# Kernel tuning notes

Measured on AMD Instinct MI355X. Metric: run time of the kernel, lower is better.

Reference implementation:

```python
import jax, jax.numpy as jnp
import numpy as np

T = 2048          # tokens (flattened batch*seq, vLLM style)
HID = 2048        # hidden_size
NH = 16           # num_heads
D_NOPE = 128
D_ROPE = 64
D_QK = D_NOPE + D_ROPE   # 192
D_V = 128
Q_LORA = 1536
KV_LORA = 512
THETA = 10000.0
EPS = 1e-6
SCALING = D_QK ** -0.5


def _rmsnorm(x, g):
    return x * jax.lax.rsqrt(jnp.mean(x * x, axis=-1, keepdims=True) + EPS) * g


def _rope(pos, x):
    # interleaved (is_neox_style=False) rotary embedding
    d = x.shape[-1]
    inv = 1.0 / (THETA ** (jnp.arange(0, d, 2, dtype=jnp.float32) / d))
    f = pos.astype(jnp.float32)[:, None] * inv          # [T, d/2]
    cos, sin = jnp.cos(f), jnp.sin(f)
    for _ in range(x.ndim - 2):                          # broadcast over heads
        cos, sin = cos[:, None], sin[:, None]
    x1, x2 = x[..., 0::2], x[..., 1::2]
    o1 = x1 * cos - x2 * sin
    o2 = x1 * sin + x2 * cos
    return jnp.stack([o1, o2], axis=-1).reshape(x.shape)


def setup_inputs() -> dict:
    key = jax.random.key(0)
    ks = jax.random.split(key, 6)
    s = 0.02
    return {
        "hidden_states": jax.random.normal(ks[0], (T, HID), jnp.float32),
        "positions": jnp.arange(T, dtype=jnp.int32),
        "w_qkv_a": jax.random.normal(ks[1], (HID, Q_LORA + KV_LORA + D_ROPE), jnp.float32) * s,
        "g_q": jnp.ones((Q_LORA,), jnp.float32),
        "w_q_b": jax.random.normal(ks[2], (Q_LORA, NH * D_QK), jnp.float32) * s,
        "g_kv": jnp.ones((KV_LORA,), jnp.float32),
        "w_kv_b": jax.random.normal(ks[3], (KV_LORA, NH * (D_NOPE + D_V)), jnp.float32) * s,
        "w_o": jax.random.normal(ks[4], (NH * D_V, HID), jnp.float32) * s,
    }


def reference(hidden_states, positions, w_qkv_a, g_q, w_q_b, g_kv, w_kv_b, w_o):
    # fused low-rank a-projection: [T, q_lora + kv_lora + rope]
    qkv_a = hidden_states @ w_qkv_a
    q_lat = qkv_a[:, :Q_LORA]
    kv_lat = qkv_a[:, Q_LORA:Q_LORA + KV_LORA]
    k_pe = qkv_a[:, Q_LORA + KV_LORA:]                   # [T, rope]

    # query path: rmsnorm -> b-projection -> [T, H, d_qk]
    q = (_rmsnorm(q_lat, g_q) @ w_q_b).reshape(T, NH, D_QK)
    q_nope, q_pe = q[..., :D_NOPE], q[..., D_NOPE:]

    # kv path: rmsnorm -> b-projection -> [T, H, nope + v]
    kv = (_rmsnorm(kv_lat, g_kv) @ w_kv_b).reshape(T, NH, D_NOPE + D_V)
    k_nope, v = kv[..., :D_NOPE], kv[..., D_NOPE:]

    q_pe = _rope(positions, q_pe)                        # [T, H, rope]
    k_pe = _rope(positions, k_pe)                        # [T, rope] shared MQA rope key

    qf = jnp.concatenate([q_nope, q_pe], axis=-1)        # [T, H, d_qk]
    kf = jnp.concatenate([k_nope, jnp.broadcast_to(k_pe[:, None, :], (T, NH, D_ROPE))], axis=-1)

    scores = jnp.einsum("thd,shd->hts", qf, kf) * SCALING   # [H, T, T]
    mask = jnp.tril(jnp.ones((T, T), dtype=bool))
    scores = jnp.where(mask, scores, jnp.finfo(scores.dtype).min)
    probs = jax.nn.softmax(scores, axis=-1)
    out = jnp.einsum("hts,shd->thd", probs, v)           # [T, H, d_v]
    return out.reshape(T, NH * D_V) @ w_o                # [T, hidden]
```

## Files before the change

### kernel.cpp

```cpp
#include <hip/hip_runtime.h>
#include <hip/hip_bf16.h>
#include <math.h>

typedef __bf16 bf16_t;
typedef __bf16 bf16x8 __attribute__((ext_vector_type(8)));
typedef float floatx4 __attribute__((ext_vector_type(4)));
typedef int intx4 __attribute__((ext_vector_type(4)));

#define T_TOK 2048
#define HID 2048
#define NH 16
#define D_NOPE 128
#define D_ROPE 64
#define D_QK 192
#define D_V 128
#define Q_LORA 1536
#define KV_LORA 512
#define QKV_N 2112
#define QKV_NPAD 2176
#define SCALING 0.07216878364870323f
#define LOG2E 1.442695041f
#define EXP_C1 (SCALING * LOG2E)
#define EXP_C2 (12.0f * LOG2E)

#define MFMA_BF16(a, b, c) __builtin_amdgcn_mfma_f32_16x16x32_bf16(a, b, c, 0, 0, 0)

__device__ __forceinline__ void gload16(const void* g, void* l) {
    __builtin_amdgcn_global_load_lds(
        (const __attribute__((address_space(1))) unsigned int*)g,
        (__attribute__((address_space(3))) unsigned int*)l, 16, 0, 0);
}

template <int MODE>
__device__ __forceinline__ void gemm_body(
    const bf16_t* __restrict__ A, const bf16_t* __restrict__ Bt,
    float* __restrict__ Cf, bf16_t* __restrict__ Cb,
    bf16_t* __restrict__ kfull, bf16_t* __restrict__ vT,
    int N, int K, int m0, int n0, bf16_t* S)
{
    bf16_t* As = S;
    bf16_t* Bs = S + 16384;
    const int tid = threadIdx.x;
    const int lane = tid & 63;
    const int w = tid >> 6;
    const int wm = w >> 1, wn = w & 1;
    const int l15 = lane & 15, quad = lane >> 4;
    const int ckey = (l15 >> 1) & 3;

    floatx4 acc[4][4] = {};

#define GSTAGE(db_, k0_)                                                                 \
    do {                                                                                 \
        _Pragma("unroll")                                                                \
        for (int it = 0; it < 4; ++it) {                                                 \
            int slot = it * 256 + tid;                                                   \
            int kk2 = slot >> 9;                                                         \
            int r = (slot >> 2) & 127;                                                   \
            int c = slot & 3;                                                            \
            int cs = c ^ ((r >> 1) & 3);                                                 \
            gload16((const char*)(A + (size_t)(m0 + r) * K + (k0_) + kk2 * 32 + cs * 8), \
                    (char*)(As + (size_t)(db_)*8192) + slot * 16);                       \
            gload16((const char*)(Bt + (size_t)(n0 + r) * K + (k0_) + kk2 * 32 + cs * 8),\
                    (char*)(Bs + (size_t)(db_)*8192) + slot * 16);                       \
        }                                                                                \
    } while (0)

    GSTAGE(0, 0);
    int db = 0;
    for (int k0 = 0; k0 < K; k0 += 64) {
        __syncthreads();
        if (k0 + 64 < K) GSTAGE(db ^ 1, k0 + 64);
        const bf16_t* Ab = As + (size_t)db * 8192;
        const bf16_t* Bb = Bs + (size_t)db * 8192;
#pragma unroll
        for (int kk2 = 0; kk2 < 2; ++kk2) {
            bf16x8 af[4], bfr[4];
#pragma unroll
            for (int mi = 0; mi < 4; ++mi)
                af[mi] = *(const bf16x8*)(Ab + kk2 * 4096 +
                                          (wm * 64 + mi * 16 + l15) * 32 +
                                          (quad ^ ckey) * 8);
#pragma unroll
            for (int ni = 0; ni < 4; ++ni)
                bfr[ni] = *(const bf16x8*)(Bb + kk2 * 4096 +
                                           (wn * 64 + ni * 16 + l15) * 32 +
                                           (quad ^ ckey) * 8);
#pragma unroll
            for (int mi = 0; mi < 4; ++mi)
#pragma unroll
                for (int ni = 0; ni < 4; ++ni)
                    acc[mi][ni] = MFMA_BF16(af[mi], bfr[ni], acc[mi][ni]);
        }
        db ^= 1;
    }
#undef GSTAGE

    if (MODE == 2) {
        const int hh = n0 >> 8;
        if ((n0 & 255) == 0) {
#pragma unroll
            for (int mi = 0; mi < 4; ++mi)
#pragma unroll
                for (int ni = 0; ni < 4; ++ni)
#pragma unroll
                    for (int r = 0; r < 4; ++r) {
                        int row = m0 + wm * 64 + mi * 16 + quad * 4 + r;
                        int dd = wn * 64 + ni * 16 + l15;
                        kfull[((size_t)hh * T_TOK + row) * 192 + dd] =
                            (bf16_t)acc[mi][ni][r];
                    }
        } else {
            __syncthreads();
            bf16_t* Tq = S;
#pragma unroll
            for (int mi = 0; mi < 4; ++mi)
#pragma unroll
                for (int ni = 0; ni < 4; ++ni)
#pragma unroll
                    for (int r = 0; r < 4; ++r) {
                        int rloc = wm * 64 + mi * 16 + quad * 4 + r;
                        int cloc = wn * 64 + ni * 16 + l15;
                        Tq[cloc * 136 + rloc] = (bf16_t)acc[mi][ni][r];
                    }
            __syncthreads();
#pragma unroll
            for (int pass = 0; pass < 8; ++pass) {
                int dcol = pass * 16 + w * 4 + quad;
                bf16x8 vv = *(const bf16x8*)(Tq + dcol * 136 + l15 * 8);
                *(bf16x8*)(vT + ((size_t)hh * 128 + dcol) * T_TOK + m0 + l15 * 8) = vv;
            }
        }
        return;
    }

#pragma unroll
    for (int mi = 0; mi < 4; ++mi)
#pragma unroll
        for (int ni = 0; ni < 4; ++ni)
#pragma unroll
            for (int r = 0; r < 4; ++r) {
                int row = m0 + wm * 64 + mi * 16 + quad * 4 + r;
                int col = n0 + wn * 64 + ni * 16 + l15;
                float v = acc[mi][ni][r];
                if (MODE == 1) {
                    Cb[(size_t)row * N + col] = (bf16_t)v;
                } else {
                    Cf[(size_t)row * N + col] = v;
                }
            }
}

template <int MODE>
__global__ __launch_bounds__(256) void gemm_mfma(
    const bf16_t* __restrict__ A, const bf16_t* __restrict__ Bt,
    float* __restrict__ Cf, bf16_t* __restrict__ Cb,
    bf16_t* __restrict__ kfull, bf16_t* __restrict__ vT,
    int M, int N, int K)
{
    __shared__ __align__(16) bf16_t S[4 * 8192];
    gemm_body<MODE>(A, Bt, Cf, Cb, kfull, vT, N, K,
                    blockIdx.y * 128, blockIdx.x * 128, S);
}

__global__ __launch_bounds__(256) void gemm_dual(
    const bf16_t* __restrict__ qn, const bf16_t* __restrict__ wqb,
    bf16_t* __restrict__ qbuf,
    const bf16_t* __restrict__ kvn, const bf16_t* __restrict__ wkvb,
    bf16_t* __restrict__ kfull, bf16_t* __restrict__ vT)
{
    __shared__ __align__(16) bf16_t S[4 * 8192];
    int id = blockIdx.x;
    if (id < 384) {
        gemm_body<1>(qn, wqb, nullptr, qbuf, nullptr, nullptr,
                     3072, Q_LORA, (id / 24) * 128, (id % 24) * 128, S);
    } else {
        int i2 = id - 384;
        gemm_body<2>(kvn, wkvb, nullptr, nullptr, kfull, vT,
                     4096, KV_LORA, (i2 / 32) * 128, (i2 % 32) * 128, S);
    }
}

__global__ void transpose_all(const float* __restrict__ w0, const float* __restrict__ w1,
                              const float* __restrict__ w2, const float* __restrict__ w3,
                              const float* __restrict__ hidden,
                              bf16_t* __restrict__ o0, bf16_t* __restrict__ o1,
                              bf16_t* __restrict__ o2, bf16_t* __restrict__ o3,
                              bf16_t* __restrict__ hbf) {
    int n0 = blockIdx.x * 32, k0 = blockIdx.y * 32;
    int tx = threadIdx.x, ty = threadIdx.y;
    if (blockIdx.z == 4) {
        if (n0 >= 2048 || k0 >= 2048) return;
        for (int i = ty; i < 32; i += 8)
            hbf[(size_t)(k0 + i) * 2048 + n0 + tx] =
                (bf16_t)hidden[(size_t)(k0 + i) * 2048 + n0 + tx];
        return;
    }
    const float* in; bf16_t* out; int K, N;
    switch (blockIdx.z) {
        case 0: in = w0; out = o0; K = 2048; N = 2112; break;
        case 1: in = w1; out = o1; K = 1536; N = 3072; break;
        case 2: in = w2; out = o2; K = 512;  N = 4096; break;
        default: in = w3; out = o3; K = 2048; N = 2048; break;
    }
    if (n0 >= N || k0 >= K) return;
    __shared__ float tile[32][33];
    for (int i = ty; i < 32; i += 8)
        tile[i][tx] = in[(size_t)(k0 + i) * N + n0 + tx];
    __syncthreads();
    for (int i = ty; i < 32; i += 8)
        out[(size_t)(n0 + i) * K + k0 + tx] = (bf16_t)tile[tx][i];
}

__global__ void mid_fuse(const float* __restrict__ qkv_a, const int* __restrict__ pos,
                         const float* __restrict__ g_q, const float* __restrict__ g_kv,
                         bf16_t* __restrict__ qn, bf16_t* __restrict__ kvn,
                         bf16_t* __restrict__ kfull, float2* __restrict__ ropet) {
    int t = blockIdx.x, tid = threadIdx.x;
    const float* x = qkv_a + (size_t)t * QKV_NPAD;
    __shared__ float red[256];
    float ss = 0.f;
    for (int c = tid; c < Q_LORA; c += 256) { float v = x[c]; ss += v * v; }
    red[tid] = ss;
    __syncthreads();
    for (int o = 128; o > 0; o >>= 1) {
        if (tid < o) red[tid] += red[tid + o];
        __syncthreads();
    }
    float rq = rsqrtf(red[0] / (float)Q_LORA + 1e-6f);
    __syncthreads();
    ss = 0.f;
    for (int c = Q_LORA + tid; c < Q_LORA + KV_LORA; c += 256) { float v = x[c]; ss += v * v; }
    red[tid] = ss;
    __syncthreads();
    for (int o = 128; o > 0; o >>= 1) {
        if (tid < o) red[tid] += red[tid + o];
        __syncthreads();
    }
    float rkv = rsqrtf(red[0] / (float)KV_LORA + 1e-6f);

    for (int c = tid; c < Q_LORA; c += 256)
        qn[(size_t)t * Q_LORA + c] = (bf16_t)(x[c] * rq * g_q[c]);
    for (int c = tid; c < KV_LORA; c += 256)
        kvn[(size_t)t * KV_LORA + c] = (bf16_t)(x[Q_LORA + c] * rkv * g_kv[c]);

    if (tid < 32) {
        int i = tid;
        double inv = pow(10000.0, -(double)(2 * i) / 64.0);
        double fd = (double)pos[t] * inv;
        float c = (float)cos(fd), s = (float)sin(fd);
        ropet[t * 32 + i] = make_float2(c, s);
        float x1 = x[Q_LORA + KV_LORA + 2 * i], x2 = x[Q_LORA + KV_LORA + 2 * i + 1];
        bf16_t v0 = (bf16_t)(x1 * c - x2 * s);
        bf16_t v1 = (bf16_t)(x1 * s + x2 * c);
#pragma unroll
        for (int h = 0; h < NH; ++h) {
            kfull[((size_t)h * T_TOK + t) * 192 + 128 + 2 * i] = v0;
            kfull[((size_t)h * T_TOK + t) * 192 + 128 + 2 * i + 1] = v1;
        }
    }
}

__global__ __launch_bounds__(256, 2) void attn_part(
    const bf16_t* __restrict__ qbuf, const bf16_t* __restrict__ kfull,
    const bf16_t* __restrict__ vT, const float2* __restrict__ ropet,
    bf16_t* __restrict__ oP0, bf16_t* __restrict__ oP1, float* __restrict__ l_part)
{
    const int id = blockIdx.x;
    const int h = id & 15;
    const int c = (id >> 4) & 3;
    const int qt = 15 - (id >> 6);
    const int q0 = qt * 128;
    const int nTile = 2 * (qt + 1);
    const int tbase = nTile >> 2, trem = nTile & 3;
    const int sz = tbase + (c < trem ? 1 : 0);
    const int sBeg = c * tbase + (c < trem ? c : trem);
    const int sEnd = sBeg + sz;
    const int unit = qt * 16 + h;
    const int tid = threadIdx.x, lane = tid & 63, w = tid >> 6;
    const int l15 = lane & 15, quad = lane >> 4;
    const int ckey = (l15 >> 1) & 3;

    __shared__ __align__(16) bf16_t kn2[2][6 * 64 * 32];
    __shared__ __align__(16) bf16_t vt2[2 * 128 * 32];
    __shared__ __align__(16) bf16_t p_s[128 * 64];

    bf16x8 qf[2][6];
#pragma unroll
    for (int st = 0; st < 2; ++st) {
        const bf16_t* qp = qbuf + (size_t)(q0 + w * 32 + st * 16 + l15) * (NH * D_QK) +
                           h * D_QK;
#pragma unroll
        for (int kk = 0; kk < 6; ++kk)
            qf[st][kk] = *(const bf16x8*)(qp + kk * 32 + quad * 8);
    }
#pragma unroll
    for (int st = 0; st < 2; ++st) {
        int t = q0 + w * 32 + st * 16 + l15;
#pragma unroll
        for (int kk = 4; kk < 6; ++kk)
#pragma unroll
            for (int p = 0; p < 4; ++p) {
                float2 cs = ropet[t * 32 + (kk - 4) * 16 + quad * 4 + p];
                float x1 = (float)qf[st][kk][2 * p], x2 = (float)qf[st][kk][2 * p + 1];
                qf[st][kk][2 * p] = (bf16_t)(x1 * cs.x - x2 * cs.y);
                qf[st][kk][2 * p + 1] = (bf16_t)(x1 * cs.y + x2 * cs.x);
            }
    }

    bf16x8 ones;
#pragma unroll
    for (int j = 0; j < 8; ++j) ones[j] = (bf16_t)1.0f;

    floatx4 o[2][8] = {};
    floatx4 lac[2] = {};
    intx4 vreg[4];

#define STAGE_KN(buf_, s0_)                                                              \
    do {                                                                                 \
        _Pragma("unroll")                                                                \
        for (int it = 0; it < 6; ++it) {                                                 \
            int slot = it * 256 + tid;                                                   \
            int kk = slot >> 8, s = (slot >> 2) & 63, cc = slot & 3;                     \
            int cs = cc ^ ((s >> 1) & 3);                                                \
            gload16((const char*)(kfull + ((size_t)h * T_TOK + (s0_) + s) * 192 +        \
                                  kk * 32 + cs * 8),                                     \
                    (char*)kn2[buf_] + slot * 16);                                       \
        }                                                                                \
    } while (0)

#define VLOAD(s0_)                                                                       \
    do {                                                                                 \
        _Pragma("unroll")                                                                \
        for (int it = 0; it < 4; ++it) {                                                 \
            int slot = it * 256 + tid;                                                   \
            int ks = slot >> 9, d = (slot >> 2) & 127, cc = slot & 3;                    \
            vreg[it] = *(const intx4*)(vT + ((size_t)h * 128 + d) * T_TOK + (s0_) +      \
                                       ks * 32 + cc * 8);                                \
        }                                                                                \
    } while (0)

#define VWRITE()                                                                         \
    do {                                                                                 \
        _Pragma("unroll")                                                                \
        for (int it = 0; it < 4; ++it) {                                                 \
            int slot = it * 256 + tid;                                                   \
            int ks = slot >> 9, d = (slot >> 2) & 127, cc = slot & 3;                    \
            *(intx4*)((char*)vt2 +                                                       \
                      (size_t)((ks * 512 + d * 4 + (cc ^ ((d >> 1) & 3))) * 16)) =       \
                vreg[it];                                                                \
        }                                                                                \
    } while (0)

    if (sz > 0) {
        VLOAD(sBeg * 64);
        STAGE_KN(0, sBeg * 64);
        VWRITE();
    }

    for (int si = sBeg; si < sEnd; ++si) {
        const int s0 = si * 64;
        const int buf = (si - sBeg) & 1;
        __syncthreads();
        if (si + 1 < sEnd) {
            VLOAD(s0 + 64);
            STAGE_KN(buf ^ 1, s0 + 64);
        }

        floatx4 s_acc[2][4] = {};
        __builtin_amdgcn_s_setprio(1);
#pragma unroll
        for (int ni = 0; ni < 4; ++ni) {
#pragma unroll
            for (int kk = 0; kk < 6; ++kk) {
                bf16x8 b = *(const bf16x8*)(kn2[buf] + kk * 2048 +
                                            (ni * 16 + l15) * 32 + (quad ^ ckey) * 8);
                s_acc[0][ni] = MFMA_BF16(qf[0][kk], b, s_acc[0][ni]);
                s_acc[1][ni] = MFMA_BF16(qf[1][kk], b, s_acc[1][ni]);
            }
        }
        __builtin_amdgcn_s_setprio(0);

        const bool diag = (si >= 2 * qt);
#pragma unroll
        for (int st = 0; st < 2; ++st)
#pragma unroll
            for (int ni = 0; ni < 4; ++ni)
#pragma unroll
                for (int r = 0; r < 4; ++r) {
                    int prow = w * 32 + st * 16 + quad * 4 + r;
                    int pcol = ni * 16 + l15;
                    float pv = exp2f(s_acc[st][ni][r] * EXP_C1 - EXP_C2);
                    if (diag && (s0 + pcol) > (q0 + prow)) pv = 0.f;
                    p_s[prow * 64 + ((((pcol >> 3) ^ (prow & 7))) << 3) + (pcol & 7)] =
                        (bf16_t)pv;
                }

        __builtin_amdgcn_s_setprio(1);
#pragma unroll
        for (int ks = 0; ks < 2; ++ks) {
            bf16x8 a0, a1;
            {
                int arow = w * 32 + l15;
                a0 = *(const bf16x8*)(p_s + arow * 64 +
                                      (((ks * 4 + quad) ^ (arow & 7)) << 3));
                arow += 16;
                a1 = *(const bf16x8*)(p_s + arow * 64 +
                                      (((ks * 4 + quad) ^ (arow & 7)) << 3));
            }
            lac[0] = MFMA_BF16(a0, ones, lac[0]);
            lac[1] = MFMA_BF16(a1, ones, lac[1]);
#pragma unroll
            for (int ni = 0; ni < 8; ++ni) {
                bf16x8 b = *(const bf16x8*)(vt2 + ks * 4096 +
                                            (ni * 16 + l15) * 32 + (quad ^ ckey) * 8);
                o[0][ni] = MFMA_BF16(a0, b, o[0][ni]);
                o[1][ni] = MFMA_BF16(a1, b, o[1][ni]);
            }
        }
        __builtin_amdgcn_s_setprio(0);

        __syncthreads();
        if (si + 1 < sEnd) VWRITE();
    }

    bf16_t* op = ((c < 2) ? oP0 : oP1) + (size_t)(unit * 2 + (c & 1)) * 128 * 128;
#pragma unroll
    for (int st = 0; st < 2; ++st) {
#pragma unroll
        for (int ni = 0; ni < 8; ++ni)
#pragma unroll
            for (int r = 0; r < 4; ++r) {
                int lrow = w * 32 + st * 16 + quad * 4 + r;
                op[(size_t)lrow * 128 + ni * 16 + l15] = (bf16_t)o[st][ni][r];
            }
        if (l15 == 0)
#pragma unroll
            for (int r = 0; r < 4; ++r) {
                int lrow = w * 32 + st * 16 + quad * 4 + r;
                l_part[((size_t)unit * 4 + c) * 128 + lrow] = lac[st][r];
            }
    }
#undef STAGE_KN
#undef VLOAD
#undef VWRITE
}

__global__ void attn_combine(const bf16_t* __restrict__ oP0,
                             const bf16_t* __restrict__ oP1,
                             const float* __restrict__ l_part,
                             bf16_t* __restrict__ attn_o)
{
    int idx = blockIdx.x * 256 + threadIdx.x;
    int t = idx >> 8, cg = idx & 255;
    int col = cg * 8;
    int h = col >> 7, d = col & 127;
    int qt = t >> 7, lrow = t & 127;
    size_t unit = (size_t)qt * 16 + h;
    const float* lp = l_part + unit * 4 * 128 + lrow;
    float inv = 1.f / (lp[0] + lp[128] + lp[256] + lp[384]);
    size_t r0 = ((unit * 2 + 0) * 128 + lrow) * 128 + d;
    size_t r1 = ((unit * 2 + 1) * 128 + lrow) * 128 + d;
    bf16x8 a0 = *(const bf16x8*)(oP0 + r0);
    bf16x8 a1 = *(const bf16x8*)(oP0 + r1);
    bf16x8 a2 = *(const bf16x8*)(oP1 + r0);
    bf16x8 a3 = *(const bf16x8*)(oP1 + r1);
    bf16x8 out;
#pragma unroll
    for (int j = 0; j < 8; ++j)
        out[j] = (bf16_t)(((float)a0[j] + (float)a1[j] + (float)a2[j] + (float)a3[j]) * inv);
    *(bf16x8*)(attn_o + (size_t)t * (NH * D_V) + col) = out;
}

extern "C" void kernel_launch(void* const* d_in, const int* in_sizes, int n_in,
                              void* d_out, int out_size, void* d_ws, size_t ws_size,
                              hipStream_t stream) {
    const float* hidden = (const float*)d_in[0];
    const int* positions = (const int*)d_in[1];
    const float* w_qkv_a = (const float*)d_in[2];
    const float* g_q = (const float*)d_in[3];
    const float* w_q_b = (const float*)d_in[4];
    const float* g_kv = (const float*)d_in[5];
    const float* w_kv_b = (const float*)d_in[6];
    const float* w_o = (const float*)d_in[7];
    float* out = (float*)d_out;

    char* p = (char*)d_ws;
    float* qkv_a = (float*)p;
    bf16_t* attn_o = (bf16_t*)p;
    p += (size_t)T_TOK * QKV_NPAD * 4;
    bf16_t* hbf = (bf16_t*)p;
    bf16_t* qn = hbf;
    bf16_t* kvn = hbf + (size_t)T_TOK * Q_LORA;
    p += (size_t)T_TOK * HID * 2;
    bf16_t* qbuf = (bf16_t*)p;  p += (size_t)T_TOK * NH * D_QK * 2;
    bf16_t* vtmp = (bf16_t*)p;  p += (size_t)T_TOK * NH * D_V * 2;
    bf16_t* kfull = (bf16_t*)p; p += (size_t)NH * T_TOK * 192 * 2;
    bf16_t* vT = (bf16_t*)p;    p += (size_t)NH * 128 * T_TOK * 2;
    bf16_t* wt_qkv_a = (bf16_t*)p; p += (size_t)QKV_NPAD * HID * 2;
    bf16_t* wt_q_b = (bf16_t*)p;   p += (size_t)3072 * Q_LORA * 2;
    bf16_t* wt_kv_b = (bf16_t*)p;  p += (size_t)4096 * KV_LORA * 2;
    bf16_t* wt_o = (bf16_t*)p;

    float2* ropet = (float2*)vtmp;
    float* l_part = (float*)((char*)vtmp + (1 << 20));
    bf16_t* oP0 = wt_qkv_a;
    bf16_t* oP1 = (bf16_t*)((char*)d_ws + (size_t)T_TOK * HID * 2);

    dim3 tb(32, 8);

    transpose_all<<<dim3(128, 64, 5), tb, 0, stream>>>(
        w_qkv_a, w_q_b, w_kv_b, w_o, hidden, wt_qkv_a, wt_q_b, wt_kv_b, wt_o, hbf);

    gemm_mfma<0><<<dim3(QKV_NPAD / 128, T_TOK / 128), 256, 0, stream>>>(
        hbf, wt_qkv_a, qkv_a, nullptr, nullptr, nullptr, T_TOK, QKV_NPAD, HID);

    mid_fuse<<<T_TOK, 256, 0, stream>>>(qkv_a, positions, g_q, g_kv, qn, kvn,
                                        kfull, ropet);

    gemm_dual<<<896, 256, 0, stream>>>(qn, wt_q_b, qbuf, kvn, wt_kv_b, kfull, vT);

    attn_part<<<1024, 256, 0, stream>>>(qbuf, kfull, vT, ropet, oP0, oP1, l_part);
    attn_combine<<<(T_TOK * 256) / 256, 256, 0, stream>>>(oP0, oP1, l_part, attn_o);

    gemm_mfma<0><<<dim3(HID / 128, T_TOK / 128), 256, 0, stream>>>(
        attn_o, wt_o, out, nullptr, nullptr, nullptr, T_TOK, HID, NH * D_V);
}
```

Baseline: 302.7 us.

## Split-K the a-projection and output GEMMs into two halves for more blocks

The qkv a-projection and the output projection GEMMs now run as split-K with two K halves launched via blockIdx.z, doubling block count to better fill the GPU's compute units. The a-projection partials are summed inside mid_fuse, which now stages the row in shared memory, and the output partials are summed by a new add_f32 kernel. Workspace buffers are reassigned to hold the second partial. This trades extra fp32 partial traffic and one extra launch for higher occupancy on grids of only 272/256 tiles.

```diff
diff --git a/kernel.cpp b/kernel.cpp
--- a/kernel.cpp
+++ b/kernel.cpp
@@ -36,7 +36,7 @@
     const bf16_t* __restrict__ A, const bf16_t* __restrict__ Bt,
     float* __restrict__ Cf, bf16_t* __restrict__ Cb,
     bf16_t* __restrict__ kfull, bf16_t* __restrict__ vT,
-    int N, int K, int m0, int n0, bf16_t* S)
+    int N, int Kloop, int Kst, int m0, int n0, bf16_t* S)
 {
     bf16_t* As = S;
     bf16_t* Bs = S + 16384;
@@ -58,18 +58,18 @@
             int r = (slot >> 2) & 127;                                                   \
             int c = slot & 3;                                                            \
             int cs = c ^ ((r >> 1) & 3);                                                 \
-            gload16((const char*)(A + (size_t)(m0 + r) * K + (k0_) + kk2 * 32 + cs * 8), \
+            gload16((const char*)(A + (size_t)(m0 + r) * Kst + (k0_) + kk2 * 32 + cs * 8),\
                     (char*)(As + (size_t)(db_)*8192) + slot * 16);                       \
-            gload16((const char*)(Bt + (size_t)(n0 + r) * K + (k0_) + kk2 * 32 + cs * 8),\
+            gload16((const char*)(Bt + (size_t)(n0 + r) * Kst + (k0_) + kk2 * 32 + cs * 8),\
                     (char*)(Bs + (size_t)(db_)*8192) + slot * 16);                       \
         }                                                                                \
     } while (0)
 
     GSTAGE(0, 0);
     int db = 0;
-    for (int k0 = 0; k0 < K; k0 += 64) {
+    for (int k0 = 0; k0 < Kloop; k0 += 64) {
         __syncthreads();
-        if (k0 + 64 < K) GSTAGE(db ^ 1, k0 + 64);
+        if (k0 + 64 < Kloop) GSTAGE(db ^ 1, k0 + 64);
         const bf16_t* Ab = As + (size_t)db * 8192;
         const bf16_t* Bb = Bs + (size_t)db * 8192;
 #pragma unroll
@@ -150,16 +150,16 @@
             }
 }
 
-template <int MODE>
-__global__ __launch_bounds__(256) void gemm_mfma(
+__global__ __launch_bounds__(256) void gemm_sk0(
     const bf16_t* __restrict__ A, const bf16_t* __restrict__ Bt,
-    float* __restrict__ Cf, bf16_t* __restrict__ Cb,
-    bf16_t* __restrict__ kfull, bf16_t* __restrict__ vT,
-    int M, int N, int K)
+    float* __restrict__ P0, float* __restrict__ P1, int N, int K)
 {
     __shared__ __align__(16) bf16_t S[4 * 8192];
-    gemm_body<MODE>(A, Bt, Cf, Cb, kfull, vT, N, K,
-                    blockIdx.y * 128, blockIdx.x * 128, S);
+    const int half = blockIdx.z;
+    const int Kh = K >> 1;
+    gemm_body<0>(A + half * Kh, Bt + half * Kh, half ? P1 : P0,
+                 nullptr, nullptr, nullptr,
+                 N, Kh, K, blockIdx.y * 128, blockIdx.x * 128, S);
 }
 
 __global__ __launch_bounds__(256) void gemm_dual(
@@ -172,12 +172,20 @@
     int id = blockIdx.x;
     if (id < 384) {
         gemm_body<1>(qn, wqb, nullptr, qbuf, nullptr, nullptr,
-                     3072, Q_LORA, (id / 24) * 128, (id % 24) * 128, S);
+                     3072, Q_LORA, Q_LORA, (id / 24) * 128, (id % 24) * 128, S);
     } else {
         int i2 = id - 384;
         gemm_body<2>(kvn, wkvb, nullptr, nullptr, kfull, vT,
-                     4096, KV_LORA, (i2 / 32) * 128, (i2 % 32) * 128, S);
-    }
+                     4096, KV_LORA, KV_LORA, (i2 / 32) * 128, (i2 % 32) * 128, S);
+    }
+}
+
+__global__ void add_f32(const float* __restrict__ a, const float* __restrict__ b,
+                        float* __restrict__ o) {
+    int i = blockIdx.x * 256 + threadIdx.x;
+    float4 va = ((const float4*)a)[i];
+    float4 vb = ((const float4*)b)[i];
+    ((float4*)o)[i] = make_float4(va.x + vb.x, va.y + vb.y, va.z + vb.z, va.w + vb.w);
 }
 
 __global__ void transpose_all(const float* __restrict__ w0, const float* __restrict__ w1,
@@ -211,15 +219,20 @@
         out[(size_t)(n0 + i) * K + k0 + tx] = (bf16_t)tile[tx][i];
 }
 
-__global__ void mid_fuse(const float* __restrict__ qkv_a, const int* __restrict__ pos,
+__global__ void mid_fuse(const float* __restrict__ p0, const float* __restrict__ p1,
+                         const int* __restrict__ pos,
                          const float* __restrict__ g_q, const float* __restrict__ g_kv,
                          bf16_t* __restrict__ qn, bf16_t* __restrict__ kvn,
                          bf16_t* __restrict__ kfull, float2* __restrict__ ropet) {
     int t = blockIdx.x, tid = threadIdx.x;
-    const float* x = qkv_a + (size_t)t * QKV_NPAD;
+    const float* x0 = p0 + (size_t)t * QKV_NPAD;
+    const float* x1 = p1 + (size_t)t * QKV_NPAD;
+    __shared__ float row[QKV_N];
     __shared__ float red[256];
     float ss = 0.f;
-    for (int c = tid; c < Q_LORA; c += 256) { float v = x[c]; ss += v * v; }
+    for (int c = tid; c < Q_LORA; c += 256) {
+        float v = x0[c] + x1[c]; row[c] = v; ss += v * v;
+    }
     red[tid] = ss;
     __syncthreads();
     for (int o = 128; o > 0; o >>= 1) {
@@ -229,7 +242,13 @@
     float rq = rsqrtf(red[0] / (float)Q_LORA + 1e-6f);
     __syncthreads();
     ss = 0.f;
-    for (int c = Q_LORA + tid; c < Q_LORA + KV_LORA; c += 256) { float v = x[c]; ss += v * v; }
+    for (int c = Q_LORA + tid; c < Q_LORA + KV_LORA; c += 256) {
+        float v = x0[c] + x1[c]; row[c] = v; ss += v * v;
+    }
+    if (tid < 64) {
+        int c = Q_LORA + KV_LORA + tid;
+        row[c] = x0[c] + x1[c];
+    }
     red[tid] = ss;
     __syncthreads();
     for (int o = 128; o > 0; o >>= 1) {
@@ -239,9 +258,9 @@
     float rkv = rsqrtf(red[0] / (float)KV_LORA + 1e-6f);
 
     for (int c = tid; c < Q_LORA; c += 256)
-        qn[(size_t)t * Q_LORA + c] = (bf16_t)(x[c] * rq * g_q[c]);
+        qn[(size_t)t * Q_LORA + c] = (bf16_t)(row[c] * rq * g_q[c]);
     for (int c = tid; c < KV_LORA; c += 256)
-        kvn[(size_t)t * KV_LORA + c] = (bf16_t)(x[Q_LORA + c] * rkv * g_kv[c]);
+        kvn[(size_t)t * KV_LORA + c] = (bf16_t)(row[Q_LORA + c] * rkv * g_kv[c]);
 
     if (tid < 32) {
         int i = tid;
@@ -249,9 +268,9 @@
         double fd = (double)pos[t] * inv;
         float c = (float)cos(fd), s = (float)sin(fd);
         ropet[t * 32 + i] = make_float2(c, s);
-        float x1 = x[Q_LORA + KV_LORA + 2 * i], x2 = x[Q_LORA + KV_LORA + 2 * i + 1];
-        bf16_t v0 = (bf16_t)(x1 * c - x2 * s);
-        bf16_t v1 = (bf16_t)(x1 * s + x2 * c);
+        float x1v = row[Q_LORA + KV_LORA + 2 * i], x2v = row[Q_LORA + KV_LORA + 2 * i + 1];
+        bf16_t v0 = (bf16_t)(x1v * c - x2v * s);
+        bf16_t v1 = (bf16_t)(x1v * s + x2v * c);
 #pragma unroll
         for (int h = 0; h < NH; ++h) {
             kfull[((size_t)h * T_TOK + t) * 192 + 128 + 2 * i] = v0;
@@ -501,27 +520,31 @@
     bf16_t* wt_kv_b = (bf16_t*)p;  p += (size_t)4096 * KV_LORA * 2;
     bf16_t* wt_o = (bf16_t*)p;
 
-    float2* ropet = (float2*)vtmp;
-    float* l_part = (float*)((char*)vtmp + (1 << 20));
+    float* g1p1 = (float*)qbuf;
+    float2* ropet = (float2*)((char*)vtmp + (7u << 20));
+    float* l_part = (float*)((char*)vtmp + (7u << 20) + (1u << 19));
     bf16_t* oP0 = wt_qkv_a;
     bf16_t* oP1 = (bf16_t*)((char*)d_ws + (size_t)T_TOK * HID * 2);
+    float* gop0 = (float*)wt_qkv_a;
+    float* gop1 = (float*)oP1;
 
     dim3 tb(32, 8);
 
     transpose_all<<<dim3(128, 64, 5), tb, 0, stream>>>(
         w_qkv_a, w_q_b, w_kv_b, w_o, hidden, wt_qkv_a, wt_q_b, wt_kv_b, wt_o, hbf);
 
-    gemm_mfma<0><<<dim3(QKV_NPAD / 128, T_TOK / 128), 256, 0, stream>>>(
-        hbf, wt_qkv_a, qkv_a, nullptr, nullptr, nullptr, T_TOK, QKV_NPAD, HID);
-
-    mid_fuse<<<T_TOK, 256, 0, stream>>>(qkv_a, positions, g_q, g_kv, qn, kvn,
-                                        kfull, ropet);
+    gemm_sk0<<<dim3(QKV_NPAD / 128, T_TOK / 128, 2), 256, 0, stream>>>(
+        hbf, wt_qkv_a, qkv_a, g1p1, QKV_NPAD, HID);
+
+    mid_fuse<<<T_TOK, 256, 0, stream>>>(qkv_a, g1p1, positions, g_q, g_kv,
+                                        qn, kvn, kfull, ropet);
 
     gemm_dual<<<896, 256, 0, stream>>>(qn, wt_q_b, qbuf, kvn, wt_kv_b, kfull, vT);
 
     attn_part<<<1024, 256, 0, stream>>>(qbuf, kfull, vT, ropet, oP0, oP1, l_part);
     attn_combine<<<(T_TOK * 256) / 256, 256, 0, stream>>>(oP0, oP1, l_part, attn_o);
 
-    gemm_mfma<0><<<dim3(HID / 128, T_TOK / 128), 256, 0, stream>>>(
-        attn_o, wt_o, out, nullptr, nullptr, nullptr, T_TOK, HID, NH * D_V);
-}
+    gemm_sk0<<<dim3(HID / 128, T_TOK / 128, 2), 256, 0, stream>>>(
+        attn_o, wt_o, gop0, gop1, HID, NH * D_V);
+    add_f32<<<(T_TOK * HID) / 1024, 256, 0, stream>>>(gop0, gop1, out);
+}
```

After: 310.0 us. 1.02x slower.

## Fuse RMSNorm into projection GEMMs via epilogue sum-of-squares and weight-folded gains

Applied to the files above, without the earlier changes.

The qkv_a GEMM now writes bf16 output and accumulates per-row sums of squares with atomics in its epilogue. The RMSNorm gain is folded into the transposed b-projection weights, and the row rsqrt scale is applied in the downstream GEMM epilogues. This removes the full normalisation pass in mid_fuse, the fp32 qkv_a round-trip and the separate qn/kvn buffers, leaving only a small rope kernel. In exchange it adds atomics and reads the unnormalised latent in bf16, which changes rounding slightly.

```diff
diff --git a/kernel.cpp b/kernel.cpp
--- a/kernel.cpp
+++ b/kernel.cpp
@@ -36,7 +36,8 @@
     const bf16_t* __restrict__ A, const bf16_t* __restrict__ Bt,
     float* __restrict__ Cf, bf16_t* __restrict__ Cb,
     bf16_t* __restrict__ kfull, bf16_t* __restrict__ vT,
-    int N, int K, int m0, int n0, bf16_t* S)
+    float* __restrict__ sqq, float* __restrict__ sqkv,
+    int N, int K, int Ast, int Bst, int m0, int n0, bf16_t* S)
 {
     bf16_t* As = S;
     bf16_t* Bs = S + 16384;
@@ -58,9 +59,9 @@
             int r = (slot >> 2) & 127;                                                   \
             int c = slot & 3;                                                            \
             int cs = c ^ ((r >> 1) & 3);                                                 \
-            gload16((const char*)(A + (size_t)(m0 + r) * K + (k0_) + kk2 * 32 + cs * 8), \
+            gload16((const char*)(A + (size_t)(m0 + r) * Ast + (k0_) + kk2 * 32 + cs * 8),\
                     (char*)(As + (size_t)(db_)*8192) + slot * 16);                       \
-            gload16((const char*)(Bt + (size_t)(n0 + r) * K + (k0_) + kk2 * 32 + cs * 8),\
+            gload16((const char*)(Bt + (size_t)(n0 + r) * Bst + (k0_) + kk2 * 32 + cs * 8),\
                     (char*)(Bs + (size_t)(db_)*8192) + slot * 16);                       \
         }                                                                                \
     } while (0)
@@ -95,33 +96,85 @@
     }
 #undef GSTAGE
 
+    if (MODE == 3) {
+#pragma unroll
+        for (int mi = 0; mi < 4; ++mi)
+#pragma unroll
+            for (int ni = 0; ni < 4; ++ni)
+#pragma unroll
+                for (int r = 0; r < 4; ++r) {
+                    int row = m0 + wm * 64 + mi * 16 + quad * 4 + r;
+                    int col = n0 + wn * 64 + ni * 16 + l15;
+                    Cb[(size_t)row * N + col] = (bf16_t)acc[mi][ni][r];
+                }
+        float* sq = (n0 + 128 <= Q_LORA) ? sqq
+                  : ((n0 >= Q_LORA && n0 + 128 <= Q_LORA + KV_LORA) ? sqkv : nullptr);
+        if (sq) {
+#pragma unroll
+            for (int mi = 0; mi < 4; ++mi)
+#pragma unroll
+                for (int r = 0; r < 4; ++r) {
+                    float s = 0.f;
+#pragma unroll
+                    for (int ni = 0; ni < 4; ++ni) {
+                        float v = acc[mi][ni][r]; s += v * v;
+                    }
+                    s += __shfl_xor(s, 1); s += __shfl_xor(s, 2);
+                    s += __shfl_xor(s, 4); s += __shfl_xor(s, 8);
+                    if (l15 == 0)
+                        atomicAdd(&sq[m0 + wm * 64 + mi * 16 + quad * 4 + r], s);
+                }
+        }
+        return;
+    }
+
+    if (MODE == 1) {
+#pragma unroll
+        for (int mi = 0; mi < 4; ++mi)
+#pragma unroll
+            for (int r = 0; r < 4; ++r) {
+                int row = m0 + wm * 64 + mi * 16 + quad * 4 + r;
+                float rq = rsqrtf(sqq[row] * (1.f / Q_LORA) + 1e-6f);
+#pragma unroll
+                for (int ni = 0; ni < 4; ++ni) {
+                    int col = n0 + wn * 64 + ni * 16 + l15;
+                    Cb[(size_t)row * N + col] = (bf16_t)(acc[mi][ni][r] * rq);
+                }
+            }
+        return;
+    }
+
     if (MODE == 2) {
         const int hh = n0 >> 8;
         if ((n0 & 255) == 0) {
 #pragma unroll
             for (int mi = 0; mi < 4; ++mi)
 #pragma unroll
-                for (int ni = 0; ni < 4; ++ni)
-#pragma unroll
-                    for (int r = 0; r < 4; ++r) {
-                        int row = m0 + wm * 64 + mi * 16 + quad * 4 + r;
+                for (int r = 0; r < 4; ++r) {
+                    int row = m0 + wm * 64 + mi * 16 + quad * 4 + r;
+                    float rkv = rsqrtf(sqkv[row] * (1.f / KV_LORA) + 1e-6f);
+#pragma unroll
+                    for (int ni = 0; ni < 4; ++ni) {
                         int dd = wn * 64 + ni * 16 + l15;
                         kfull[((size_t)hh * T_TOK + row) * 192 + dd] =
-                            (bf16_t)acc[mi][ni][r];
+                            (bf16_t)(acc[mi][ni][r] * rkv);
                     }
+                }
         } else {
             __syncthreads();
             bf16_t* Tq = S;
 #pragma unroll
             for (int mi = 0; mi < 4; ++mi)
 #pragma unroll
-                for (int ni = 0; ni < 4; ++ni)
-#pragma unroll
-                    for (int r = 0; r < 4; ++r) {
-                        int rloc = wm * 64 + mi * 16 + quad * 4 + r;
+                for (int r = 0; r < 4; ++r) {
+                    int rloc = wm * 64 + mi * 16 + quad * 4 + r;
+                    float rkv = rsqrtf(sqkv[m0 + rloc] * (1.f / KV_LORA) + 1e-6f);
+#pragma unroll
+                    for (int ni = 0; ni < 4; ++ni) {
                         int cloc = wn * 64 + ni * 16 + l15;
-                        Tq[cloc * 136 + rloc] = (bf16_t)acc[mi][ni][r];
+                        Tq[cloc * 136 + rloc] = (bf16_t)(acc[mi][ni][r] * rkv);
                     }
+                }
             __syncthreads();
 #pragma unroll
             for (int pass = 0; pass < 8; ++pass) {
@@ -141,122 +194,104 @@
             for (int r = 0; r < 4; ++r) {
                 int row = m0 + wm * 64 + mi * 16 + quad * 4 + r;
                 int col = n0 + wn * 64 + ni * 16 + l15;
-                float v = acc[mi][ni][r];
-                if (MODE == 1) {
-                    Cb[(size_t)row * N + col] = (bf16_t)v;
-                } else {
-                    Cf[(size_t)row * N + col] = v;
-                }
-            }
-}
-
-template <int MODE>
-__global__ __launch_bounds__(256) void gemm_mfma(
-    const bf16_t* __restrict__ A, const bf16_t* __restrict__ Bt,
-    float* __restrict__ Cf, bf16_t* __restrict__ Cb,
-    bf16_t* __restrict__ kfull, bf16_t* __restrict__ vT,
-    int M, int N, int K)
+                Cf[(size_t)row * N + col] = acc[mi][ni][r];
+            }
+}
+
+__global__ __launch_bounds__(256) void gemm_qkv_a(
+    const bf16_t* __restrict__ hbf, const bf16_t* __restrict__ wt,
+    bf16_t* __restrict__ qkv_ab, float* __restrict__ sqq, float* __restrict__ sqkv)
 {
     __shared__ __align__(16) bf16_t S[4 * 8192];
-    gemm_body<MODE>(A, Bt, Cf, Cb, kfull, vT, N, K,
-                    blockIdx.y * 128, blockIdx.x * 128, S);
+    gemm_body<3>(hbf, wt, nullptr, qkv_ab, nullptr, nullptr, sqq, sqkv,
+                 QKV_NPAD, HID, HID, HID, blockIdx.y * 128, blockIdx.x * 128, S);
 }
 
 __global__ __launch_bounds__(256) void gemm_dual(
-    const bf16_t* __restrict__ qn, const bf16_t* __restrict__ wqb,
-    bf16_t* __restrict__ qbuf,
-    const bf16_t* __restrict__ kvn, const bf16_t* __restrict__ wkvb,
-    bf16_t* __restrict__ kfull, bf16_t* __restrict__ vT)
+    const bf16_t* __restrict__ qkv_ab, const bf16_t* __restrict__ wqb,
+    bf16_t* __restrict__ qbuf, const bf16_t* __restrict__ wkvb,
+    bf16_t* __restrict__ kfull, bf16_t* __restrict__ vT,
+    float* __restrict__ sqq, float* __restrict__ sqkv)
 {
     __shared__ __align__(16) bf16_t S[4 * 8192];
     int id = blockIdx.x;
     if (id < 384) {
-        gemm_body<1>(qn, wqb, nullptr, qbuf, nullptr, nullptr,
-                     3072, Q_LORA, (id / 24) * 128, (id % 24) * 128, S);
+        gemm_body<1>(qkv_ab, wqb, nullptr, qbuf, nullptr, nullptr, sqq, nullptr,
+                     3072, Q_LORA, QKV_NPAD, Q_LORA,
+                     (id / 24) * 128, (id % 24) * 128, S);
     } else {
         int i2 = id - 384;
-        gemm_body<2>(kvn, wkvb, nullptr, nullptr, kfull, vT,
-                     4096, KV_LORA, (i2 / 32) * 128, (i2 % 32) * 128, S);
-    }
+        gemm_body<2>(qkv_ab + Q_LORA, wkvb, nullptr, nullptr, kfull, vT,
+                     nullptr, sqkv,
+                     4096, KV_LORA, QKV_NPAD, KV_LORA,
+                     (i2 / 32) * 128, (i2 % 32) * 128, S);
+    }
+}
+
+__global__ __launch_bounds__(256) void gemm_out(
+    const bf16_t* __restrict__ attn_o, const bf16_t* __restrict__ wto,
+    float* __restrict__ out)
+{
+    __shared__ __align__(16) bf16_t S[4 * 8192];
+    gemm_body<0>(attn_o, wto, out, nullptr, nullptr, nullptr, nullptr, nullptr,
+                 HID, HID, HID, HID, blockIdx.y * 128, blockIdx.x * 128, S);
 }
 
 __global__ void transpose_all(const float* __restrict__ w0, const float* __restrict__ w1,
                               const float* __restrict__ w2, const float* __restrict__ w3,
                               const float* __restrict__ hidden,
+                              const float* __restrict__ g_q, const float* __restrict__ g_kv,
                               bf16_t* __restrict__ o0, bf16_t* __restrict__ o1,
                               bf16_t* __restrict__ o2, bf16_t* __restrict__ o3,
-                              bf16_t* __restrict__ hbf) {
+                              bf16_t* __restrict__ hbf, float* __restrict__ sqbuf) {
     int n0 = blockIdx.x * 32, k0 = blockIdx.y * 32;
     int tx = threadIdx.x, ty = threadIdx.y;
     if (blockIdx.z == 4) {
+        if (blockIdx.x == 0 && blockIdx.y == 0) {
+            int t = ty * 32 + tx;
+            for (int j = t; j < 4096; j += 256) sqbuf[j] = 0.f;
+        }
         if (n0 >= 2048 || k0 >= 2048) return;
         for (int i = ty; i < 32; i += 8)
             hbf[(size_t)(k0 + i) * 2048 + n0 + tx] =
                 (bf16_t)hidden[(size_t)(k0 + i) * 2048 + n0 + tx];
         return;
     }
-    const float* in; bf16_t* out; int K, N;
+    const float* in; bf16_t* out; const float* g; int K, N;
     switch (blockIdx.z) {
-        case 0: in = w0; out = o0; K = 2048; N = 2112; break;
-        case 1: in = w1; out = o1; K = 1536; N = 3072; break;
-        case 2: in = w2; out = o2; K = 512;  N = 4096; break;
-        default: in = w3; out = o3; K = 2048; N = 2048; break;
+        case 0: in = w0; out = o0; g = nullptr; K = 2048; N = 2112; break;
+        case 1: in = w1; out = o1; g = g_q;     K = 1536; N = 3072; break;
+        case 2: in = w2; out = o2; g = g_kv;    K = 512;  N = 4096; break;
+        default: in = w3; out = o3; g = nullptr; K = 2048; N = 2048; break;
     }
     if (n0 >= N || k0 >= K) return;
     __shared__ float tile[32][33];
     for (int i = ty; i < 32; i += 8)
         tile[i][tx] = in[(size_t)(k0 + i) * N + n0 + tx];
     __syncthreads();
+    float gk = g ? g[k0 + tx] : 1.f;
     for (int i = ty; i < 32; i += 8)
-        out[(size_t)(n0 + i) * K + k0 + tx] = (bf16_t)tile[tx][i];
-}
-
-__global__ void mid_fuse(const float* __restrict__ qkv_a, const int* __restrict__ pos,
-                         const float* __restrict__ g_q, const float* __restrict__ g_kv,
-                         bf16_t* __restrict__ qn, bf16_t* __restrict__ kvn,
-                         bf16_t* __restrict__ kfull, float2* __restrict__ ropet) {
+        out[(size_t)(n0 + i) * K + k0 + tx] = (bf16_t)(tile[tx][i] * gk);
+}
+
+__global__ void mid_fuse_lite(const bf16_t* __restrict__ qkv_ab,
+                              const int* __restrict__ pos,
+                              float2* __restrict__ ropet, bf16_t* __restrict__ kfull) {
     int t = blockIdx.x, tid = threadIdx.x;
-    const float* x = qkv_a + (size_t)t * QKV_NPAD;
-    __shared__ float red[256];
-    float ss = 0.f;
-    for (int c = tid; c < Q_LORA; c += 256) { float v = x[c]; ss += v * v; }
-    red[tid] = ss;
-    __syncthreads();
-    for (int o = 128; o > 0; o >>= 1) {
-        if (tid < o) red[tid] += red[tid + o];
-        __syncthreads();
-    }
-    float rq = rsqrtf(red[0] / (float)Q_LORA + 1e-6f);
-    __syncthreads();
-    ss = 0.f;
-    for (int c = Q_LORA + tid; c < Q_LORA + KV_LORA; c += 256) { float v = x[c]; ss += v * v; }
-    red[tid] = ss;
-    __syncthreads();
-    for (int o = 128; o > 0; o >>= 1) {
-        if (tid < o) red[tid] += red[tid + o];
-        __syncthreads();
-    }
-    float rkv = rsqrtf(red[0] / (float)KV_LORA + 1e-6f);
-
-    for (int c = tid; c < Q_LORA; c += 256)
-        qn[(size_t)t * Q_LORA + c] = (bf16_t)(x[c] * rq * g_q[c]);
-    for (int c = tid; c < KV_LORA; c += 256)
-        kvn[(size_t)t * KV_LORA + c] = (bf16_t)(x[Q_LORA + c] * rkv * g_kv[c]);
-
-    if (tid < 32) {
-        int i = tid;
-        double inv = pow(10000.0, -(double)(2 * i) / 64.0);
-        double fd = (double)pos[t] * inv;
-        float c = (float)cos(fd), s = (float)sin(fd);
-        ropet[t * 32 + i] = make_float2(c, s);
-        float x1 = x[Q_LORA + KV_LORA + 2 * i], x2 = x[Q_LORA + KV_LORA + 2 * i + 1];
-        bf16_t v0 = (bf16_t)(x1 * c - x2 * s);
-        bf16_t v1 = (bf16_t)(x1 * s + x2 * c);
-#pragma unroll
-        for (int h = 0; h < NH; ++h) {
-            kfull[((size_t)h * T_TOK + t) * 192 + 128 + 2 * i] = v0;
-            kfull[((size_t)h * T_TOK + t) * 192 + 128 + 2 * i + 1] = v1;
-        }
+    if (tid >= 32) return;
+    int i = tid;
+    double inv = pow(10000.0, -(double)(2 * i) / 64.0);
+    double fd = (double)pos[t] * inv;
+    float c = (float)cos(fd), s = (float)sin(fd);
+    ropet[t * 32 + i] = make_float2(c, s);
+    float x1 = (float)qkv_ab[(size_t)t * QKV_NPAD + Q_LORA + KV_LORA + 2 * i];
+    float x2 = (float)qkv_ab[(size_t)t * QKV_NPAD + Q_LORA + KV_LORA + 2 * i + 1];
+    bf16_t v0 = (bf16_t)(x1 * c - x2 * s);
+    bf16_t v1 = (bf16_t)(x1 * s + x2 * c);
+#pragma unroll
+    for (int h = 0; h < NH; ++h) {
+        kfull[((size_t)h * T_TOK + t) * 192 + 128 + 2 * i] = v0;
+        kfull[((size_t)h * T_TOK + t) * 192 + 128 + 2 * i + 1] = v1;
     }
 }
 
@@ -485,12 +520,10 @@
     float* out = (float*)d_out;
 
     char* p = (char*)d_ws;
-    float* qkv_a = (float*)p;
+    bf16_t* qkv_ab = (bf16_t*)p;
     bf16_t* attn_o = (bf16_t*)p;
     p += (size_t)T_TOK * QKV_NPAD * 4;
     bf16_t* hbf = (bf16_t*)p;
-    bf16_t* qn = hbf;
-    bf16_t* kvn = hbf + (size_t)T_TOK * Q_LORA;
     p += (size_t)T_TOK * HID * 2;
     bf16_t* qbuf = (bf16_t*)p;  p += (size_t)T_TOK * NH * D_QK * 2;
     bf16_t* vtmp = (bf16_t*)p;  p += (size_t)T_TOK * NH * D_V * 2;
@@ -503,25 +536,27 @@
 
     float2* ropet = (float2*)vtmp;
     float* l_part = (float*)((char*)vtmp + (1 << 20));
+    float* sq_q = (float*)((char*)vtmp + (2 << 20));
+    float* sq_kv = sq_q + 2048;
     bf16_t* oP0 = wt_qkv_a;
     bf16_t* oP1 = (bf16_t*)((char*)d_ws + (size_t)T_TOK * HID * 2);
 
     dim3 tb(32, 8);
 
     transpose_all<<<dim3(128, 64, 5), tb, 0, stream>>>(
-        w_qkv_a, w_q_b, w_kv_b, w_o, hidden, wt_qkv_a, wt_q_b, wt_kv_b, wt_o, hbf);
-
-    gemm_mfma<0><<<dim3(QKV_NPAD / 128, T_TOK / 128), 256, 0, stream>>>(
-        hbf, wt_qkv_a, qkv_a, nullptr, nullptr, nullptr, T_TOK, QKV_NPAD, HID);
-
-    mid_fuse<<<T_TOK, 256, 0, stream>>>(qkv_a, positions, g_q, g_kv, qn, kvn,
-                                        kfull, ropet);
-
-    gemm_dual<<<896, 256, 0, stream>>>(qn, wt_q_b, qbuf, kvn, wt_kv_b, kfull, vT);
+        w_qkv_a, w_q_b, w_kv_b, w_o, hidden, g_q, g_kv,
+        wt_qkv_a, wt_q_b, wt_kv_b, wt_o, hbf, sq_q);
+
+    gemm_qkv_a<<<dim3(QKV_NPAD / 128, T_TOK / 128), 256, 0, stream>>>(
+        hbf, wt_qkv_a, qkv_ab, sq_q, sq_kv);
+
+    mid_fuse_lite<<<T_TOK, 64, 0, stream>>>(qkv_ab, positions, ropet, kfull);
+
+    gemm_dual<<<896, 256, 0, stream>>>(qkv_ab, wt_q_b, qbuf, wt_kv_b, kfull, vT,
+                                       sq_q, sq_kv);
 
     attn_part<<<1024, 256, 0, stream>>>(qbuf, kfull, vT, ropet, oP0, oP1, l_part);
     attn_combine<<<(T_TOK * 256) / 256, 256, 0, stream>>>(oP0, oP1, l_part, attn_o);
 
-    gemm_mfma<0><<<dim3(HID / 128, T_TOK / 128), 256, 0, stream>>>(
-        attn_o, wt_o, out, nullptr, nullptr, nullptr, T_TOK, HID, NH * D_V);
-}
+    gemm_out<<<dim3(HID / 128, T_TOK / 128), 256, 0, stream>>>(attn_o, wt_o, out);
+}
```

After: 302.6 us. About the same (-0.0%).
